# Kernel tuning notes

Hardware: AMD Instinct MI355X
Metric: run time of the kernel (lower is better)

## Reference

```python
import jax, jax.numpy as jnp
import numpy as np
from jax import lax

NH, K, V, TOPK = 8, 64, 64, 4  # n_heads, key_size, val_size, SparseAttention top_k(=3+1)
EPS = 1e-7
BN_EPS = 1e-5


def conv1x1(x, w, b):
    # x: [B,C,H,W], w: [O,C] -> [B,O,H,W]
    return jnp.einsum('oc,bchw->bohw', w, x) + b[None, :, None, None]


def conv3x3(x, w, b):
    y = lax.conv_general_dilated(x, w, (1, 1), 'SAME',
                                 dimension_numbers=('NCHW', 'OIHW', 'NCHW'))
    return y + b[None, :, None, None]


def batchnorm(x, g, b):
    # training-mode BN over (N,H,W), biased variance (matches torch BatchNorm2d in train)
    m = jnp.mean(x, axis=(0, 2, 3), keepdims=True)
    v = jnp.var(x, axis=(0, 2, 3), keepdims=True)
    return (x - m) * lax.rsqrt(v + BN_EPS) * g[None, :, None, None] + b[None, :, None, None]


def to_flat(y, d):
    # [B, NH*d, H, W] -> [B*H*W*NH, d]
    B, _, H, W = y.shape
    return y.reshape(B, NH, d, H, W).transpose(0, 3, 4, 1, 2).reshape(B * H * W * NH, d)


def setup_inputs() -> dict:
    key = jax.random.key(0)
    ks = jax.random.split(key, 16)
    L, C, B, H, W = 4, 256, 8, 32, 32
    KH, VH = K * NH, V * NH
    s = 0.02
    return {
        'x': jax.random.normal(ks[0], (B, C, H, W), jnp.float32),
        'kw': jax.random.normal(ks[1], (L, KH, C), jnp.float32) * s,
        'kb': jax.random.normal(ks[2], (L, KH), jnp.float32) * s,
        'qw': jax.random.normal(ks[3], (L, KH, C), jnp.float32) * s,
        'qb': jax.random.normal(ks[4], (L, KH), jnp.float32) * s,
        'vw': jax.random.normal(ks[5], (L, VH, C), jnp.float32) * s,
        'vb': jax.random.normal(ks[6], (L, VH), jnp.float32) * s,
        'ow1': jax.random.normal(ks[7], (L, C, VH, 3, 3), jnp.float32) * s,
        'ob1': jax.random.normal(ks[8], (L, C), jnp.float32) * s,
        'bn_g': jnp.ones((L, C), jnp.float32),
        'bn_b': jnp.zeros((L, C), jnp.float32),
        'ow2': jax.random.normal(ks[9], (L, C, C, 3, 3), jnp.float32) * s,
        'ob2': jax.random.normal(ks[10], (L, C), jnp.float32) * s,
        'gammas': jax.random.normal(ks[11], (L,), jnp.float32),
    }


def reference(x, kw, kb, qw, qb, vw, vb, ow1, ob1, bn_g, bn_b, ow2, ob2, gammas):
    B, C, H, W = x.shape
    L = kw.shape[0]
    temp = jnp.asarray(np.power(K, 0.5), x.dtype)  # concentration=0.5
    keys, vals = [], []
    for l in range(L):  # structurally distinct layers: growing key/val list
        keys.append(to_flat(conv1x1(x, kw[l], kb[l]), K))  # [N,K]
        vals.append(to_flat(conv1x1(x, vw[l], vb[l]), V))  # [N,V]
        q = to_flat(conv1x1(x, qw[l], qb[l]), K)           # [N,K]
        kt = jnp.stack(keys + [jnp.zeros_like(keys[0])], axis=1)  # [N,T,K] zero key appended
        vt = jnp.stack(vals + [jnp.zeros_like(vals[0])], axis=1)  # [N,T,V]
        scores = jnp.einsum('nk,ntk->nt', q / temp, kt)
        attn = jax.nn.softmax(scores, axis=-1)
        T = attn.shape[1]
        if T > TOPK:  # SparseAttention: topk threshold, clamp, renormalize
            delta = lax.top_k(attn, TOPK)[0][:, -1] + EPS
            wgt = jnp.maximum(attn - delta[:, None], 0.0)
            attn = wgt / (jnp.sum(wgt, axis=1, keepdims=True) + EPS)
        o = jnp.einsum('nt,ntv->nv', attn, vt)  # [N,V]
        o = o.reshape(B, H, W, NH * V).transpose(0, 3, 1, 2)  # [B, NH*V, H, W]
        h1 = jax.nn.relu(batchnorm(conv3x3(o, ow1[l], ob1[l]), bn_g[l], bn_b[l]))
        h2 = conv3x3(h1, ow2[l], ob2[l])
        x = x + h2 * gammas[l]
    return x
```

## Files before the change

### kernel.cpp

```cpp
#include <hip/hip_runtime.h>


typedef __attribute__((ext_vector_type(8))) short short8;
typedef __attribute__((ext_vector_type(4))) float f32x4;
typedef __attribute__((ext_vector_type(2))) float f32x2;
typedef __attribute__((ext_vector_type(4))) unsigned short ushort4_t;
typedef __attribute__((ext_vector_type(4))) unsigned int uint4_t;

#define NTOK 65536
#define NPIX 8192

__device__ __forceinline__ float bf2f(unsigned short u) {
  unsigned int v = ((unsigned int)u) << 16;
  float f; __builtin_memcpy(&f, &v, 4); return f;
}
__device__ __forceinline__ unsigned short f2bf(float f) {
  unsigned int u; __builtin_memcpy(&u, &f, 4);
  u = (u + 0x7FFFu + ((u >> 16) & 1u)) >> 16;
  return (unsigned short)u;
}
__device__ __forceinline__ float blo(unsigned int u) {
  unsigned int v = u << 16; float f; __builtin_memcpy(&f, &v, 4); return f;
}
__device__ __forceinline__ float bhi(unsigned int u) {
  unsigned int v = u & 0xFFFF0000u; float f; __builtin_memcpy(&f, &v, 4); return f;
}

__device__ __forceinline__ void gl_lds16(const unsigned short* g, const unsigned short* l) {
  __builtin_amdgcn_global_load_lds(
      (const __attribute__((address_space(1))) unsigned int*)g,
      (__attribute__((address_space(3))) unsigned int*)l, 16, 0, 0);
}

__global__ void k_prep(const float* __restrict__ kw, const float* __restrict__ vw,
                       const float* __restrict__ qw, const float* __restrict__ ow1,
                       const float* __restrict__ ow2, const float* __restrict__ kb,
                       const float* __restrict__ vb, const float* __restrict__ qb,
                       unsigned short* __restrict__ wkqv, unsigned short* __restrict__ w1,
                       unsigned short* __restrict__ w2, float* __restrict__ biascat) {
  long i = (long)blockIdx.x * 256 + threadIdx.x;
  if (i < 1572864) {
    int idx = (int)(i & 131071); int sl = (int)(i >> 17); int slot = sl % 3, l = sl / 3;
    const float* s = slot == 0 ? kw : slot == 1 ? vw : qw;
    wkqv[i] = f2bf(s[(size_t)l * 131072 + idx]);
    return;
  }
  i -= 1572864;
  if (i < 4718592) {
    int c = (int)(i % 512), tap = (int)((i / 512) % 9); long m = i / 4608;
    w1[i] = f2bf(ow1[(m * 512 + c) * 9 + tap]);
    return;
  }
  i -= 4718592;
  if (i < 2359296) {
    int c = (int)(i % 256), tap = (int)((i / 256) % 9); long m = i / 2304;
    w2[i] = f2bf(ow2[(m * 256 + c) * 9 + tap]);
    return;
  }
  i -= 2359296;
  if (i < 6144) {
    int o = (int)(i & 511); int sl = (int)(i >> 9); int slot = sl % 3, l = sl / 3;
    const float* s = slot == 0 ? kb : slot == 1 ? vb : qb;
    biascat[i] = s[l * 512 + o];
  }
}

__global__ __launch_bounds__(256) void k_x2cl(const float* __restrict__ src,
                                              unsigned short* __restrict__ dst) {
  __shared__ unsigned short t[64][68];
  const int hw0 = blockIdx.x * 64, b = blockIdx.y;
  const int tid = threadIdx.x;
  for (int cc = 0; cc < 4; cc++) {
    __syncthreads();
    {
      const int px = tid & 63, c = tid >> 6;
      #pragma unroll
      for (int i = 0; i < 16; i++)
        t[px][c + i * 4] = f2bf(src[((size_t)b * 256 + cc * 64 + c + i * 4) * 1024 + hw0 + px]);
    }
    __syncthreads();
    {
      const int px = tid >> 2, c0 = (tid & 3) * 16;
      unsigned short* dp = dst + ((size_t)b * 1024 + hw0 + px) * 256 + cc * 64 + c0;
      short8 v0, v1;
      #pragma unroll
      for (int i = 0; i < 8; i++) { v0[i] = (short)t[px][c0 + i]; v1[i] = (short)t[px][c0 + 8 + i]; }
      *(short8*)dp = v0; *(short8*)(dp + 8) = v1;
    }
  }
}

__global__ __launch_bounds__(256) void k_zero_borders(unsigned int* __restrict__ opad,
                                                      unsigned int* __restrict__ h1pad) {
  const int idx = blockIdx.x;
  const int b = idx / 132, i = idx % 132;
  int y, x;
  if (i < 34) { y = 0; x = i; }
  else if (i < 68) { y = 33; x = i - 34; }
  else { const int j = i - 68; y = 1 + (j >> 1); x = (j & 1) * 33; }
  const size_t pix = (size_t)b * 1156 + y * 34 + x;
  opad[pix * 256 + threadIdx.x] = 0u;
  if (threadIdx.x < 128) h1pad[pix * 128 + threadIdx.x] = 0u;
}

template<int MODE, int NSTEP, int KDIM, int CIN>
__global__ __launch_bounds__(256) void k_gemm(
    const unsigned short* __restrict__ W,
    const unsigned short* __restrict__ act,
    const float* __restrict__ bias,
    int l,
    unsigned short* __restrict__ ktok, unsigned short* __restrict__ vtok,
    unsigned short* __restrict__ qtok,
    unsigned short* __restrict__ pout) {
  __shared__ unsigned short sm[2][2][8192];

  const int bid = blockIdx.x;
  int m0, b, pix0, s;
  if constexpr (MODE == 0) {
    const int xcd = bid & 7, li = bid >> 3;
    const int nt = xcd * 8 + (li & 7);
    m0 = (li >> 3) * 128; s = 0;
    b = nt >> 3; pix0 = (nt & 7) * 128;
  } else {
    const int xcd = bid & 7, li = bid >> 3;
    const int nt = xcd * 8 + (li & 7);
    const int r = li >> 3;
    m0 = (r & 1) * 128; s = r >> 1;
    b = nt >> 3; pix0 = (nt & 7) * 128;
  }
  constexpr int SW = (MODE == 1) ? 128 : 64;

  const int tid = threadIdx.x;
  const int wid = tid >> 6, lane = tid & 63;
  const int lr = lane & 15, lg = lane >> 4;
  const int m_off = (wid >> 1) * 64, n_off = (wid & 1) * 64;

  const unsigned short* gA[4];
  const unsigned short* gB[4];
  #pragma unroll
  for (int j = 0; j < 4; j++) {
    const int o = (wid * 4 + j) * 512 + lane * 8;
    const int row = o >> 6;
    const int ksw = (((o >> 3) & 7) ^ (row & 7)) * 8;
    gA[j] = W + (size_t)(m0 + row) * KDIM + (MODE ? s * SW : 0) + ksw;
    if constexpr (MODE == 0) {
      gB[j] = act + ((size_t)b * 1024 + pix0 + row) * 256 + ksw;
    } else {
      const int pix = pix0 + row, py = pix >> 5, px = pix & 31;
      gB[j] = act + (size_t)b * 1156 * CIN + ((size_t)py * 34 + px) * CIN + s * SW + ksw;
    }
  }

  auto offA = [&](int st) -> int {
    if constexpr (MODE == 0) return st * 64;
    else if constexpr (MODE == 1) return (st >> 1) * 512 + (st & 1) * 64;
    else return st * 256;
  };
  auto offB = [&](int st) -> int {
    if constexpr (MODE == 0) return st * 64;
    else if constexpr (MODE == 1) {
      const int tap = st >> 1, dy = tap / 3, dx = tap - dy * 3;
      return (dy * 34 + dx) * 512 + (st & 1) * 64;
    } else {
      const int dy = st / 3, dx = st - dy * 3;
      return (dy * 34 + dx) * 256;
    }
  };
  auto STAGE = [&](int bf, int st) {
    const int oa = offA(st), ob = offB(st);
    #pragma unroll
    for (int j = 0; j < 4; j++) gl_lds16(gA[j] + oa, &sm[bf][0][(wid * 4 + j) * 512]);
    #pragma unroll
    for (int j = 0; j < 4; j++) gl_lds16(gB[j] + ob, &sm[bf][1][(wid * 4 + j) * 512]);
  };

  f32x4 acc[4][4] = {};

  STAGE(0, 0);
  __syncthreads();
  #pragma unroll
  for (int st = 0; st < NSTEP; st++) {
    if (st + 1 < NSTEP) STAGE((st + 1) & 1, st + 1);
    const int cur = st & 1;
    #pragma unroll
    for (int ks = 0; ks < 2; ks++) {
      short8 af[4], bfr[4];
      #pragma unroll
      for (int i = 0; i < 4; i++) {
        const int ra = m_off + i * 16 + lr;
        af[i] = *(const short8*)&sm[cur][0][ra * 64 + (((ks * 4 + lg) ^ (ra & 7)) * 8)];
        const int rb = n_off + i * 16 + lr;
        bfr[i] = *(const short8*)&sm[cur][1][rb * 64 + (((ks * 4 + lg) ^ (rb & 7)) * 8)];
      }
      #pragma unroll
      for (int i = 0; i < 4; i++)
        #pragma unroll
        for (int jn = 0; jn < 4; jn++)
          acc[i][jn] = __builtin_amdgcn_mfma_f32_16x16x32_bf16(af[i], bfr[jn], acc[i][jn], 0, 0, 0);
    }
    __syncthreads();
  }

  if constexpr (MODE == 0) {
    #pragma unroll
    for (int mi = 0; mi < 4; mi++) {
      const int mb = m0 + m_off + mi * 16 + lg * 4;
      const int tensor = mb >> 9, head = (mb >> 6) & 7, d0 = mb & 63;
      unsigned short* dst = (tensor == 0) ? ktok + (size_t)l * NTOK * 64
                          : (tensor == 1) ? vtok + (size_t)l * NTOK * 64 : qtok;
      const float b0 = bias[mb], b1 = bias[mb + 1], b2 = bias[mb + 2], b3 = bias[mb + 3];
      #pragma unroll
      for (int ni = 0; ni < 4; ni++) {
        const int n = pix0 + n_off + ni * 16 + lr;
        ushort4_t pk;
        pk[0] = f2bf(acc[mi][ni][0] + b0); pk[1] = f2bf(acc[mi][ni][1] + b1);
        pk[2] = f2bf(acc[mi][ni][2] + b2); pk[3] = f2bf(acc[mi][ni][3] + b3);
        *(ushort4_t*)&dst[(((size_t)b * 1024 + n) * 8 + head) * 64 + d0] = pk;
      }
    }
  } else {
    #pragma unroll
    for (int mi = 0; mi < 4; mi++) {
      const int mb = m0 + m_off + mi * 16 + lg * 4;
      unsigned short* orow = pout + (size_t)(s * 256 + mb) * 8192 + (size_t)b * 1024 + pix0;
      #pragma unroll
      for (int ni = 0; ni < 4; ni++) {
        const int n = n_off + ni * 16 + lr;
        #pragma unroll
        for (int r = 0; r < 4; r++) orow[(size_t)r * 8192 + n] = f2bf(acc[mi][ni][r]);
      }
    }
  }
}

template<int L>
__global__ __launch_bounds__(256) void k_attn(const unsigned int* __restrict__ q_tok,
                                              const unsigned int* __restrict__ k_tok,
                                              const unsigned int* __restrict__ v_tok,
                                              unsigned int* __restrict__ opad) {
  constexpr int T = L + 2;
  const int lane = threadIdx.x & 63, wid = threadIdx.x >> 6;
  const int ti = lane >> 2, dq = lane & 3;
  const int token = blockIdx.x * 64 + wid * 16 + ti;
  const size_t rowq = (size_t)token * 32 + dq * 8;

  unsigned int q[8];
  *(uint4_t*)&q[0] = *(const uint4_t*)(q_tok + rowq);
  *(uint4_t*)&q[4] = *(const uint4_t*)(q_tok + rowq + 4);
  float qf[16];
  #pragma unroll
  for (int j = 0; j < 8; j++) {
    qf[2 * j]     = blo(q[j]) * 0.125f;
    qf[2 * j + 1] = bhi(q[j]) * 0.125f;
  }

  float s[T];
  s[T - 1] = 0.0f;
  #pragma unroll
  for (int t = 0; t <= L; t++) {
    const unsigned int* kp = k_tok + (size_t)t * (NTOK * 32) + rowq;
    unsigned int kk[8];
    *(uint4_t*)&kk[0] = *(const uint4_t*)kp;
    *(uint4_t*)&kk[4] = *(const uint4_t*)(kp + 4);
    float p = 0.0f;
    #pragma unroll
    for (int j = 0; j < 8; j++) {
      p = fmaf(qf[2 * j], blo(kk[j]), p);
      p = fmaf(qf[2 * j + 1], bhi(kk[j]), p);
    }
    p += __shfl_xor(p, 1);
    p += __shfl_xor(p, 2);
    s[t] = p;
  }

  float mx = s[0];
  #pragma unroll
  for (int t = 1; t < T; t++) mx = fmaxf(mx, s[t]);
  float attn[T], sum = 0.0f;
  #pragma unroll
  for (int t = 0; t < T; t++) { attn[t] = __expf(s[t] - mx); sum += attn[t]; }
  const float inv = 1.0f / sum;
  #pragma unroll
  for (int t = 0; t < T; t++) attn[t] *= inv;

  if constexpr (T == 5) {
    float m1 = attn[0], m2 = 1e30f;
    #pragma unroll
    for (int t = 1; t < 5; t++) {
      const float a = attn[t];
      const float nm1 = fminf(m1, a);
      m2 = fminf(m2, fmaxf(m1, a));
      m1 = nm1;
    }
    const float delta = m2 + 1e-7f;
    float ws = 0.0f;
    #pragma unroll
    for (int t = 0; t < 5; t++) { attn[t] = fmaxf(attn[t] - delta, 0.0f); ws += attn[t]; }
    const float r = 1.0f / (ws + 1e-7f);
    #pragma unroll
    for (int t = 0; t < 5; t++) attn[t] *= r;
  }

  float o[16];
  #pragma unroll
  for (int i = 0; i < 16; i++) o[i] = 0.0f;
  #pragma unroll
  for (int t = 0; t <= L; t++) {
    const unsigned int* vp = v_tok + (size_t)t * (NTOK * 32) + rowq;
    unsigned int vv[8];
    *(uint4_t*)&vv[0] = *(const uint4_t*)vp;
    *(uint4_t*)&vv[4] = *(const uint4_t*)(vp + 4);
    const float a = attn[t];
    #pragma unroll
    for (int j = 0; j < 8; j++) {
      o[2 * j]     = fmaf(a, blo(vv[j]), o[2 * j]);
      o[2 * j + 1] = fmaf(a, bhi(vv[j]), o[2 * j + 1]);
    }
  }

  unsigned int po[8];
  #pragma unroll
  for (int j = 0; j < 8; j++) {
    unsigned int r;
    asm("v_cvt_pk_bf16_f32 %0, %1, %2" : "=v"(r) : "v"(o[2 * j]), "v"(o[2 * j + 1]));
    po[j] = r;
  }
  const int head = token & 7, pix = token >> 3;
  const int b = pix >> 10, hw = pix & 1023, y = hw >> 5, x = hw & 31;
  unsigned int* dp = opad +
      (((size_t)b * 1156 + (y + 1) * 34 + (x + 1)) * 512 + head * 64 + dq * 16) / 2;
  *(uint4_t*)dp = *(uint4_t*)&po[0];
  *(uint4_t*)(dp + 4) = *(uint4_t*)&po[4];
}

__global__ __launch_bounds__(256) void k_comb_stats(const unsigned int* __restrict__ p,
    const float* __restrict__ bias1, const float* __restrict__ g, const float* __restrict__ bta,
    unsigned int* __restrict__ h1c, float* __restrict__ stats) {
  const int c = blockIdx.x, tid = threadIdx.x;
  const float bs = bias1[c];
  const unsigned int* P0 = p + (size_t)c * 4096;
  unsigned int* H = h1c + (size_t)c * 4096;
  float s = 0.0f, ss = 0.0f;
  #pragma unroll
  for (int k2 = 0; k2 < 4; k2++) {
    const int j = (k2 * 256 + tid) * 4;
    uint4_t a0 = *(const uint4_t*)(P0 + j);
    uint4_t a1 = *(const uint4_t*)(P0 + 1048576 + j);
    uint4_t a2 = *(const uint4_t*)(P0 + 2097152 + j);
    uint4_t a3 = *(const uint4_t*)(P0 + 3145728 + j);
    uint4_t o;
    #pragma unroll
    for (int e = 0; e < 4; e++) {
      const float vl = blo(a0[e]) + blo(a1[e]) + blo(a2[e]) + blo(a3[e]) + bs;
      const float vh = bhi(a0[e]) + bhi(a1[e]) + bhi(a2[e]) + bhi(a3[e]) + bs;
      s += vl + vh; ss += vl * vl + vh * vh;
      o[e] = (unsigned int)f2bf(vl) | ((unsigned int)f2bf(vh) << 16);
    }
    *(uint4_t*)(H + j) = o;
  }
  #pragma unroll
  for (int o2 = 32; o2 > 0; o2 >>= 1) { s += __shfl_xor(s, o2); ss += __shfl_xor(ss, o2); }
  __shared__ float rs[4], rss[4];
  const int wid = tid >> 6, lane = tid & 63;
  if (lane == 0) { rs[wid] = s; rss[wid] = ss; }
  __syncthreads();
  if (tid == 0) {
    const float S = rs[0] + rs[1] + rs[2] + rs[3];
    const float SS = rss[0] + rss[1] + rss[2] + rss[3];
    const float m = S * (1.0f / 8192.0f);
    const float var = SS * (1.0f / 8192.0f) - m * m;
    const float A = g[c] * rsqrtf(var + 1e-5f);
    stats[c] = A;
    stats[256 + c] = bta[c] - m * A;
  }
}

__global__ __launch_bounds__(512) void k_bn_relu_pad(const unsigned int* __restrict__ h1c,
    const float* __restrict__ stats, unsigned short* __restrict__ hpad) {
  __shared__ unsigned short t[32][264];
  const int hw0 = blockIdx.x * 32, b = blockIdx.y, tid = threadIdx.x;
  const int u = tid & 15, cg = tid >> 4;
  const int base = ((b * 1024 + hw0) >> 1);
  #pragma unroll
  for (int i = 0; i < 8; i++) {
    const int ch = i * 32 + cg;
    const float A = stats[ch], Bt = stats[256 + ch];
    const unsigned int a = h1c[(size_t)ch * 4096 + base + u];
    t[2 * u][ch]     = f2bf(fmaxf(blo(a) * A + Bt, 0.0f));
    t[2 * u + 1][ch] = f2bf(fmaxf(bhi(a) * A + Bt, 0.0f));
  }
  __syncthreads();
  const int px = tid >> 4, c0 = (tid & 15) * 16;
  const int y = hw0 >> 5, x = hw0 & 31;
  unsigned short* dp = hpad + ((size_t)b * 1156 + (y + 1) * 34 + (x + px + 1)) * 256 + c0;
  short8 v0, v1;
  #pragma unroll
  for (int i = 0; i < 8; i++) { v0[i] = (short)t[px][c0 + i]; v1[i] = (short)t[px][c0 + 8 + i]; }
  *(short8*)dp = v0; *(short8*)(dp + 8) = v1;
}

__global__ __launch_bounds__(512) void k_comb2(const unsigned int* __restrict__ p,
    const float* __restrict__ bias2, const float* __restrict__ gamma_p, int last,
    float* __restrict__ xacc, unsigned short* __restrict__ xcl) {
  __shared__ unsigned short t[32][264];
  const int hw0 = blockIdx.x * 32, b = blockIdx.y, tid = threadIdx.x;
  const int u = tid & 15, cg = tid >> 4;
  const float gmm = gamma_p[0];
  const int base = ((b * 1024 + hw0) >> 1);
  #pragma unroll
  for (int i = 0; i < 8; i++) {
    const int ch = i * 32 + cg;
    const float bs = bias2[ch];
    const size_t j = (size_t)ch * 4096 + base + u;
    const unsigned int a0 = p[j];
    const unsigned int a1 = p[j + 1048576];
    const unsigned int a2 = p[j + 2097152];
    const unsigned int a3 = p[j + 3145728];
    const float vl = blo(a0) + blo(a1) + blo(a2) + blo(a3) + bs;
    const float vh = bhi(a0) + bhi(a1) + bhi(a2) + bhi(a3) + bs;
    float* X = xacc + ((size_t)b * 256 + ch) * 1024 + hw0 + 2 * u;
    f32x2 xv = *(const f32x2*)X;
    const float xl = xv[0] + gmm * vl;
    const float xh = xv[1] + gmm * vh;
    f32x2 xw = {xl, xh};
    *(f32x2*)X = xw;
    t[2 * u][ch]     = f2bf(xl);
    t[2 * u + 1][ch] = f2bf(xh);
  }
  __syncthreads();
  if (!last) {
    const int px = tid >> 4, c0 = (tid & 15) * 16;
    unsigned short* dp = xcl + ((size_t)b * 1024 + hw0 + px) * 256 + c0;
    short8 v0, v1;
    #pragma unroll
    for (int i = 0; i < 8; i++) { v0[i] = (short)t[px][c0 + i]; v1[i] = (short)t[px][c0 + 8 + i]; }
    *(short8*)dp = v0; *(short8*)(dp + 8) = v1;
  }
}

extern "C" void kernel_launch(void* const* d_in, const int* in_sizes, int n_in,
                              void* d_out, int out_size, void* d_ws, size_t ws_size,
                              hipStream_t stream) {
  (void)in_sizes; (void)n_in; (void)out_size;
  const float* x_in   = (const float*)d_in[0];
  const float* kw     = (const float*)d_in[1];
  const float* kb     = (const float*)d_in[2];
  const float* qw     = (const float*)d_in[3];
  const float* qb     = (const float*)d_in[4];
  const float* vw     = (const float*)d_in[5];
  const float* vb     = (const float*)d_in[6];
  const float* ow1    = (const float*)d_in[7];
  const float* ob1    = (const float*)d_in[8];
  const float* bn_g   = (const float*)d_in[9];
  const float* bn_b   = (const float*)d_in[10];
  const float* ow2    = (const float*)d_in[11];
  const float* ob2    = (const float*)d_in[12];
  const float* gammas = (const float*)d_in[13];

  char* ws = (char*)d_ws;
  size_t off = 0;
  auto alloc = [&](size_t bytes) -> void* {
    void* pp = ws + off;
    off += (bytes + 255) & ~(size_t)255;
    return pp;
  };
  unsigned short* xcl     = (unsigned short*)alloc((size_t)NPIX * 256 * 2);
  unsigned short* k_tok   = (unsigned short*)alloc((size_t)4 * NTOK * 64 * 2);
  unsigned short* v_tok   = (unsigned short*)alloc((size_t)4 * NTOK * 64 * 2);
  unsigned short* q_tok   = (unsigned short*)alloc((size_t)NTOK * 64 * 2);
  unsigned short* opad    = (unsigned short*)alloc((size_t)8 * 1156 * 512 * 2);
  unsigned int*   h1c     = (unsigned int*)alloc((size_t)256 * 4096 * 4);
  unsigned short* h1pad   = (unsigned short*)alloc((size_t)8 * 1156 * 256 * 2);
  unsigned short* p1      = (unsigned short*)alloc((size_t)4 * 256 * 8192 * 2);
  float*          stats   = (float*)alloc(512 * 4);
  unsigned short* wkqv    = (unsigned short*)alloc((size_t)4 * 3 * 512 * 256 * 2);
  unsigned short* w1bf    = (unsigned short*)alloc((size_t)1024 * 4608 * 2);
  unsigned short* w2bf    = (unsigned short*)alloc((size_t)1024 * 2304 * 2);
  float*          biascat = (float*)alloc((size_t)6144 * 4);
  if (off > ws_size) return;

  float* xacc = (float*)d_out;

  k_zero_borders<<<1056, 256, 0, stream>>>((unsigned int*)opad, (unsigned int*)h1pad);
  hipMemcpyAsync(xacc, x_in, (size_t)NPIX * 256 * 4, hipMemcpyDeviceToDevice, stream);
  k_prep<<<33816, 256, 0, stream>>>(kw, vw, qw, ow1, ow2, kb, vb, qb,
                                    wkqv, w1bf, w2bf, biascat);
  k_x2cl<<<dim3(16, 8), 256, 0, stream>>>(x_in, xcl);

  for (int l = 0; l < 4; l++) {
    k_gemm<0, 4, 256, 256><<<768, 256, 0, stream>>>(
        wkqv + (size_t)l * 3 * 512 * 256, xcl, biascat + l * 1536, l,
        k_tok, v_tok, q_tok, nullptr);
    const unsigned int* qt = (const unsigned int*)q_tok;
    const unsigned int* kt = (const unsigned int*)k_tok;
    const unsigned int* vt = (const unsigned int*)v_tok;
    unsigned int* op = (unsigned int*)opad;
    switch (l) {
      case 0: k_attn<0><<<1024, 256, 0, stream>>>(qt, kt, vt, op); break;
      case 1: k_attn<1><<<1024, 256, 0, stream>>>(qt, kt, vt, op); break;
      case 2: k_attn<2><<<1024, 256, 0, stream>>>(qt, kt, vt, op); break;
      default: k_attn<3><<<1024, 256, 0, stream>>>(qt, kt, vt, op); break;
    }
    k_gemm<1, 18, 4608, 512><<<512, 256, 0, stream>>>(
        w1bf + (size_t)l * 256 * 4608, opad, nullptr, l,
        nullptr, nullptr, nullptr, p1);
    k_comb_stats<<<256, 256, 0, stream>>>((const unsigned int*)p1, ob1 + l * 256,
                                          bn_g + l * 256, bn_b + l * 256, h1c, stats);
    k_bn_relu_pad<<<dim3(32, 8), 512, 0, stream>>>(h1c, stats, h1pad);
    k_gemm<2, 9, 2304, 256><<<512, 256, 0, stream>>>(
        w2bf + (size_t)l * 256 * 2304, h1pad, nullptr, l,
        nullptr, nullptr, nullptr, p1);
    k_comb2<<<dim3(32, 8), 512, 0, stream>>>((const unsigned int*)p1, ob2 + l * 256,
                                             gammas + l, (l == 3) ? 1 : 0, xacc, xcl);
  }
}
```

Before: 366.0 us.

## Fold border zeroing and x copy into prep kernels, single-buffer QKV GEMM, widen stats

Border zeroing of the padded buffers moves into k_prep, and the device-to-device copy of x into the output accumulator moves into k_x2cl, which now writes the fp32 value as it reads it. This removes one kernel launch and one memcpy. The QKV projection GEMM now uses a single LDS buffer (NBUF=1) instead of double buffering, which cuts shared memory and may raise occupancy but loses the load/compute overlap. k_comb_stats moves to 512 threads with fewer loop iterations per thread.

```diff
diff --git a/kernel.cpp b/kernel.cpp
--- a/kernel.cpp
+++ b/kernel.cpp
@@ -37,7 +37,8 @@
                        const float* __restrict__ ow2, const float* __restrict__ kb,
                        const float* __restrict__ vb, const float* __restrict__ qb,
                        unsigned short* __restrict__ wkqv, unsigned short* __restrict__ w1,
-                       unsigned short* __restrict__ w2, float* __restrict__ biascat) {
+                       unsigned short* __restrict__ w2, float* __restrict__ biascat,
+                       unsigned int* __restrict__ opad_u32, unsigned int* __restrict__ h1pad_u32) {
   long i = (long)blockIdx.x * 256 + threadIdx.x;
   if (i < 1572864) {
     int idx = (int)(i & 131071); int sl = (int)(i >> 17); int slot = sl % 3, l = sl / 3;
@@ -62,10 +63,31 @@
     int o = (int)(i & 511); int sl = (int)(i >> 9); int slot = sl % 3, l = sl / 3;
     const float* s = slot == 0 ? kb : slot == 1 ? vb : qb;
     biascat[i] = s[l * 512 + o];
+    return;
+  }
+  i -= 6144;
+  auto border_pix = [](int pidx) -> size_t {
+    const int b = pidx / 132, t = pidx % 132;
+    int y, x;
+    if (t < 34) { y = 0; x = t; }
+    else if (t < 68) { y = 33; x = t - 34; }
+    else { const int j = t - 68; y = 1 + (j >> 1); x = (j & 1) * 33; }
+    return (size_t)b * 1156 + y * 34 + x;
+  };
+  if (i < 270336) {
+    const int pidx = (int)(i >> 8), c = (int)(i & 255);
+    opad_u32[border_pix(pidx) * 256 + c] = 0u;
+    return;
+  }
+  i -= 270336;
+  if (i < 135168) {
+    const int pidx = (int)(i >> 7), c = (int)(i & 127);
+    h1pad_u32[border_pix(pidx) * 128 + c] = 0u;
   }
 }
 
 __global__ __launch_bounds__(256) void k_x2cl(const float* __restrict__ src,
+                                              float* __restrict__ xacc,
                                               unsigned short* __restrict__ dst) {
   __shared__ unsigned short t[64][68];
   const int hw0 = blockIdx.x * 64, b = blockIdx.y;
@@ -75,8 +97,12 @@
     {
       const int px = tid & 63, c = tid >> 6;
       #pragma unroll
-      for (int i = 0; i < 16; i++)
-        t[px][c + i * 4] = f2bf(src[((size_t)b * 256 + cc * 64 + c + i * 4) * 1024 + hw0 + px]);
+      for (int i = 0; i < 16; i++) {
+        const size_t idx = ((size_t)b * 256 + cc * 64 + c + i * 4) * 1024 + hw0 + px;
+        const float v = src[idx];
+        xacc[idx] = v;
+        t[px][c + i * 4] = f2bf(v);
+      }
     }
     __syncthreads();
     {
@@ -90,20 +116,7 @@
   }
 }
 
-__global__ __launch_bounds__(256) void k_zero_borders(unsigned int* __restrict__ opad,
-                                                      unsigned int* __restrict__ h1pad) {
-  const int idx = blockIdx.x;
-  const int b = idx / 132, i = idx % 132;
-  int y, x;
-  if (i < 34) { y = 0; x = i; }
-  else if (i < 68) { y = 33; x = i - 34; }
-  else { const int j = i - 68; y = 1 + (j >> 1); x = (j & 1) * 33; }
-  const size_t pix = (size_t)b * 1156 + y * 34 + x;
-  opad[pix * 256 + threadIdx.x] = 0u;
-  if (threadIdx.x < 128) h1pad[pix * 128 + threadIdx.x] = 0u;
-}
-
-template<int MODE, int NSTEP, int KDIM, int CIN>
+template<int MODE, int NSTEP, int KDIM, int CIN, int NBUF>
 __global__ __launch_bounds__(256) void k_gemm(
     const unsigned short* __restrict__ W,
     const unsigned short* __restrict__ act,
@@ -112,7 +125,7 @@
     unsigned short* __restrict__ ktok, unsigned short* __restrict__ vtok,
     unsigned short* __restrict__ qtok,
     unsigned short* __restrict__ pout) {
-  __shared__ unsigned short sm[2][2][8192];
+  __shared__ unsigned short sm[NBUF][2][8192];
 
   const int bid = blockIdx.x;
   int m0, b, pix0, s;
@@ -173,15 +186,7 @@
     #pragma unroll
     for (int j = 0; j < 4; j++) gl_lds16(gB[j] + ob, &sm[bf][1][(wid * 4 + j) * 512]);
   };
-
-  f32x4 acc[4][4] = {};
-
-  STAGE(0, 0);
-  __syncthreads();
-  #pragma unroll
-  for (int st = 0; st < NSTEP; st++) {
-    if (st + 1 < NSTEP) STAGE((st + 1) & 1, st + 1);
-    const int cur = st & 1;
+  auto COMPUTE = [&](int cur, f32x4 (*acc)[4]) {
     #pragma unroll
     for (int ks = 0; ks < 2; ks++) {
       short8 af[4], bfr[4];
@@ -198,7 +203,27 @@
         for (int jn = 0; jn < 4; jn++)
           acc[i][jn] = __builtin_amdgcn_mfma_f32_16x16x32_bf16(af[i], bfr[jn], acc[i][jn], 0, 0, 0);
     }
+  };
+
+  f32x4 acc[4][4] = {};
+
+  if constexpr (NBUF == 2) {
+    STAGE(0, 0);
     __syncthreads();
+    #pragma unroll
+    for (int st = 0; st < NSTEP; st++) {
+      if (st + 1 < NSTEP) STAGE((st + 1) & 1, st + 1);
+      COMPUTE(st & 1, acc);
+      __syncthreads();
+    }
+  } else {
+    #pragma unroll
+    for (int st = 0; st < NSTEP; st++) {
+      if (st) __syncthreads();
+      STAGE(0, st);
+      __syncthreads();
+      COMPUTE(0, acc);
+    }
   }
 
   if constexpr (MODE == 0) {
@@ -333,7 +358,7 @@
   *(uint4_t*)(dp + 4) = *(uint4_t*)&po[4];
 }
 
-__global__ __launch_bounds__(256) void k_comb_stats(const unsigned int* __restrict__ p,
+__global__ __launch_bounds__(512) void k_comb_stats(const unsigned int* __restrict__ p,
     const float* __restrict__ bias1, const float* __restrict__ g, const float* __restrict__ bta,
     unsigned int* __restrict__ h1c, float* __restrict__ stats) {
   const int c = blockIdx.x, tid = threadIdx.x;
@@ -342,8 +367,8 @@
   unsigned int* H = h1c + (size_t)c * 4096;
   float s = 0.0f, ss = 0.0f;
   #pragma unroll
-  for (int k2 = 0; k2 < 4; k2++) {
-    const int j = (k2 * 256 + tid) * 4;
+  for (int k2 = 0; k2 < 2; k2++) {
+    const int j = (k2 * 512 + tid) * 4;
     uint4_t a0 = *(const uint4_t*)(P0 + j);
     uint4_t a1 = *(const uint4_t*)(P0 + 1048576 + j);
     uint4_t a2 = *(const uint4_t*)(P0 + 2097152 + j);
@@ -360,13 +385,14 @@
   }
   #pragma unroll
   for (int o2 = 32; o2 > 0; o2 >>= 1) { s += __shfl_xor(s, o2); ss += __shfl_xor(ss, o2); }
-  __shared__ float rs[4], rss[4];
+  __shared__ float rs[8], rss[8];
   const int wid = tid >> 6, lane = tid & 63;
   if (lane == 0) { rs[wid] = s; rss[wid] = ss; }
   __syncthreads();
   if (tid == 0) {
-    const float S = rs[0] + rs[1] + rs[2] + rs[3];
-    const float SS = rss[0] + rss[1] + rss[2] + rss[3];
+    float S = 0.0f, SS = 0.0f;
+    #pragma unroll
+    for (int w = 0; w < 8; w++) { S += rs[w]; SS += rss[w]; }
     const float m = S * (1.0f / 8192.0f);
     const float var = SS * (1.0f / 8192.0f) - m * m;
     const float A = g[c] * rsqrtf(var + 1e-5f);
@@ -481,14 +507,13 @@
 
   float* xacc = (float*)d_out;
 
-  k_zero_borders<<<1056, 256, 0, stream>>>((unsigned int*)opad, (unsigned int*)h1pad);
-  hipMemcpyAsync(xacc, x_in, (size_t)NPIX * 256 * 4, hipMemcpyDeviceToDevice, stream);
-  k_prep<<<33816, 256, 0, stream>>>(kw, vw, qw, ow1, ow2, kb, vb, qb,
-                                    wkqv, w1bf, w2bf, biascat);
-  k_x2cl<<<dim3(16, 8), 256, 0, stream>>>(x_in, xcl);
+  k_prep<<<35400, 256, 0, stream>>>(kw, vw, qw, ow1, ow2, kb, vb, qb,
+                                    wkqv, w1bf, w2bf, biascat,
+                                    (unsigned int*)opad, (unsigned int*)h1pad);
+  k_x2cl<<<dim3(16, 8), 256, 0, stream>>>(x_in, xacc, xcl);
 
   for (int l = 0; l < 4; l++) {
-    k_gemm<0, 4, 256, 256><<<768, 256, 0, stream>>>(
+    k_gemm<0, 4, 256, 256, 1><<<768, 256, 0, stream>>>(
         wkqv + (size_t)l * 3 * 512 * 256, xcl, biascat + l * 1536, l,
         k_tok, v_tok, q_tok, nullptr);
     const unsigned int* qt = (const unsigned int*)q_tok;
@@ -501,13 +526,13 @@
       case 2: k_attn<2><<<1024, 256, 0, stream>>>(qt, kt, vt, op); break;
       default: k_attn<3><<<1024, 256, 0, stream>>>(qt, kt, vt, op); break;
     }
-    k_gemm<1, 18, 4608, 512><<<512, 256, 0, stream>>>(
+    k_gemm<1, 18, 4608, 512, 2><<<512, 256, 0, stream>>>(
         w1bf + (size_t)l * 256 * 4608, opad, nullptr, l,
         nullptr, nullptr, nullptr, p1);
-    k_comb_stats<<<256, 256, 0, stream>>>((const unsigned int*)p1, ob1 + l * 256,
+    k_comb_stats<<<256, 512, 0, stream>>>((const unsigned int*)p1, ob1 + l * 256,
                                           bn_g + l * 256, bn_b + l * 256, h1c, stats);
     k_bn_relu_pad<<<dim3(32, 8), 512, 0, stream>>>(h1c, stats, h1pad);
-    k_gemm<2, 9, 2304, 256><<<512, 256, 0, stream>>>(
+    k_gemm<2, 9, 2304, 256, 2><<<512, 256, 0, stream>>>(
         w2bf + (size_t)l * 256 * 2304, h1pad, nullptr, l,
         nullptr, nullptr, nullptr, p1);
     k_comb2<<<dim3(32, 8), 512, 0, stream>>>((const unsigned int*)p1, ob2 + l * 256,
```

After: 353.1 us. 3.5% less time.
